# Kernel optimization log

Hardware: AMD Instinct MI355X
Metric: run time of the kernel (lower is better)

## Reference

```python
import jax, jax.numpy as jnp
import numpy as np

B, L, HID = 4, 4096, 1024
H, D = 16, 64  # num_heads, head_dim


def setup_inputs() -> dict:
    key = jax.random.key(0)
    ks = jax.random.split(key, 5)
    s = 1.0 / np.sqrt(HID)
    mk = lambda k: jax.random.uniform(k, (HID, HID), minval=-s, maxval=s, dtype=jnp.float32)
    return {
        "x": jax.random.normal(ks[0], (B, L, HID), dtype=jnp.float32),
        "Wq": mk(ks[1]), "bq": jnp.zeros((HID,), jnp.float32),
        "Wk": mk(ks[2]), "bk": jnp.zeros((HID,), jnp.float32),
        "Wv": mk(ks[3]), "bv": jnp.zeros((HID,), jnp.float32),
        "Wo": mk(ks[4]), "bo": jnp.zeros((HID,), jnp.float32),
    }


def reference(x, Wq, bq, Wk, bk, Wv, bv, Wo, bo):
    Bx, Lx, _ = x.shape
    # projections (weights stored [in, out])
    q = (x @ Wq + bq).reshape(Bx, Lx, H, D)
    k = (x @ Wk + bk).reshape(Bx, Lx, H, D)
    v = (x @ Wv + bv).reshape(Bx, Lx, H, D)
    # Single window (L <= window_size): torch matmul batches over (B, L) and
    # contracts head_dim -> per-token head-to-head scores [B, L, H, H].
    scores = jnp.einsum('blhd,bled->blhe', q, k) / np.sqrt(D).astype(np.float32)
    probs = jax.nn.softmax(scores, axis=-1)
    out = jnp.einsum('blhe,bled->blhd', probs, v).reshape(Bx, Lx, HID)
    return out @ Wo + bo
```

## Files before the change

### kernel.cpp

```cpp
#include <hip/hip_runtime.h>
#include <stdint.h>


typedef __attribute__((ext_vector_type(8))) short short8;
typedef __attribute__((ext_vector_type(4))) float floatx4;
typedef __attribute__((address_space(1))) unsigned int gu32;
typedef __attribute__((address_space(3))) unsigned int lu32;

#define HID 1024
#define MTOK 16384
#define WELEM (HID * HID)
#define XELEM (MTOK * HID)

#define SBAR() __builtin_amdgcn_s_barrier()
#define WAITLGKM() do { asm volatile("s_waitcnt lgkmcnt(0)" ::: "memory"); \
                        __builtin_amdgcn_sched_barrier(0); } while (0)
#define VMCNT(n) do { asm volatile("s_waitcnt vmcnt(" #n ")" ::: "memory"); \
                      __builtin_amdgcn_sched_barrier(0); } while (0)

__device__ __forceinline__ unsigned short f2bf(float f) {
  union { float f; uint32_t u; } v; v.f = f;
  uint32_t u = v.u;
  u += 0x7fffu + ((u >> 16) & 1u);
  return (unsigned short)(u >> 16);
}

__global__ __launch_bounds__(256) void cvt_x_kernel(const float* __restrict__ x,
                                                    unsigned short* __restrict__ xb) {
  const int idx = blockIdx.x * 256 + threadIdx.x;
  float4 v = ((const float4*)x)[idx];
  ushort4 o;
  o.x = f2bf(v.x); o.y = f2bf(v.y); o.z = f2bf(v.z); o.w = f2bf(v.w);
  ((ushort4*)xb)[idx] = o;
}

__global__ __launch_bounds__(256) void cvt_w_kernel(const float* __restrict__ W0,
                                                    const float* __restrict__ W1,
                                                    const float* __restrict__ W2,
                                                    const float* __restrict__ W3,
                                                    unsigned short* __restrict__ WT) {
  const float* W = (blockIdx.z == 0) ? W0 : (blockIdx.z == 1) ? W1
                   : (blockIdx.z == 2) ? W2 : W3;
  unsigned short* out = WT + (size_t)blockIdx.z * WELEM;
  __shared__ float tile[64][65];
  const int t = threadIdx.x;
  const int n0 = blockIdx.x * 64, k0 = blockIdx.y * 64;
#pragma unroll
  for (int i = 0; i < 4; i++) {
    const int row = i * 16 + (t >> 4);
    const int col = (t & 15) * 4;
    float4 v = *(const float4*)&W[(size_t)(k0 + row) * HID + n0 + col];
    tile[row][col] = v.x; tile[row][col + 1] = v.y;
    tile[row][col + 2] = v.z; tile[row][col + 3] = v.w;
  }
  __syncthreads();
#pragma unroll
  for (int i = 0; i < 4; i++) {
    const int n = i * 16 + (t >> 4);
    const int k = (t & 15) * 4;
    ushort4 o;
    o.x = f2bf(tile[k][n]);     o.y = f2bf(tile[k + 1][n]);
    o.z = f2bf(tile[k + 2][n]); o.w = f2bf(tile[k + 3][n]);
    *(ushort4*)&out[(size_t)(n0 + n) * HID + k0 + k] = o;
  }
}

template <bool QKV>
__global__ __launch_bounds__(512, 2) void gemm256(
    const unsigned short* __restrict__ A,
    const unsigned short* __restrict__ BTb,
    const float* __restrict__ b0, const float* __restrict__ b1,
    const float* __restrict__ b2,
    void* __restrict__ Cv)
{
  __shared__ short8 smem_[131072 / 16];
  char* smem = (char*)smem_;

  constexpr int R = QKV ? 3 : 1;
  const int bid = blockIdx.x;
  const int xcd = bid & 7;
  const int j = bid >> 3;
  const int nb0 = j >> 3;
  const int mb = xcd * 8 + (j & 7);
  const int m0 = mb * 256;
  const int cb = nb0 * 256;

  const unsigned short* BT0 = QKV ? BTb : (BTb + (size_t)3 * WELEM);

  const int t_ = threadIdx.x;
  const int wv = t_ >> 6, lane = t_ & 63;
  const int quad = lane >> 4, r16 = lane & 15;
  const int wm = wv >> 2, wn = wv & 3;

  const int srow = wv * 16 + (lane >> 2);
  const int scol = ((lane & 3) ^ ((lane >> 3) & 3)) * 8;
  const unsigned short* Ag = A + (size_t)(m0 + srow) * HID + scol;
  const unsigned short* Bg = BT0 + (size_t)(cb + srow) * HID + scol;

  const int qsw = (quad ^ ((r16 >> 1) & 3)) << 4;
  const char* Ard = smem + wm * 16384 + r16 * 64 + qsw;
  const char* Brd = smem + 32768 + (wn >> 1) * 16384 + ((wn & 1) * 64 + r16) * 64 + qsw;

  floatx4 acc[8][4] = {};

  auto stageA = [&](int h, int tt) {
    const unsigned short* s = Ag + (size_t)h * 128 * HID + tt * 64;
    char* d = smem + ((tt & 1) << 16) + h * 16384 + wv * 1024;
    __builtin_amdgcn_global_load_lds((const gu32*)s,        (lu32*)d,          16, 0, 0);
    __builtin_amdgcn_global_load_lds((const gu32*)(s + 32), (lu32*)(d + 8192), 16, 0, 0);
  };
  auto stageB = [&](int h, int tt) {
    const unsigned short* s = Bg + (size_t)h * 128 * HID + tt * 64;
    char* d = smem + ((tt & 1) << 16) + 32768 + h * 16384 + wv * 1024;
    __builtin_amdgcn_global_load_lds((const gu32*)s,        (lu32*)d,          16, 0, 0);
    __builtin_amdgcn_global_load_lds((const gu32*)(s + 32), (lu32*)(d + 8192), 16, 0, 0);
  };

  const int NT = HID / 64;

  short8 alo[4][2], ahi[4][2];
  short8 b01[2][2], b23[2][2];

  stageA(0, 0); stageA(1, 0); stageB(0, 0); stageB(1, 0);
  VMCNT(0);
  SBAR();
#pragma unroll
  for (int ks = 0; ks < 2; ++ks)
#pragma unroll
    for (int mi = 0; mi < 4; ++mi)
      alo[mi][ks] = *(const short8*)(Ard + ks * 8192 + mi * 1024);

  for (int r = 0; r < R; ++r) {
    for (int t = 0; t < NT; ++t) {
      const int bufb = (t & 1) << 16;
      const int nxtb = bufb ^ 0x10000;
      const bool more = (t + 1 < NT);

      if (more) { stageA(0, t + 1); VMCNT(2); } else { VMCNT(0); }
      SBAR();
#pragma unroll
      for (int ks = 0; ks < 2; ++ks)
#pragma unroll
        for (int ni = 0; ni < 2; ++ni)
          b01[ni][ks] = *(const short8*)(Brd + bufb + ks * 8192 + ni * 1024);
#pragma unroll
      for (int ks = 0; ks < 2; ++ks)
#pragma unroll
        for (int ni = 0; ni < 2; ++ni)
          b23[ni][ks] = *(const short8*)(Brd + bufb + ks * 8192 + (2 + ni) * 1024);
      __builtin_amdgcn_s_setprio(1);
#pragma unroll
      for (int ks = 0; ks < 2; ++ks)
#pragma unroll
        for (int mi = 0; mi < 4; ++mi)
#pragma unroll
          for (int ni = 0; ni < 2; ++ni)
            acc[mi][ni] = __builtin_amdgcn_mfma_f32_16x16x32_bf16(alo[mi][ks], b01[ni][ks], acc[mi][ni], 0, 0, 0);
      __builtin_amdgcn_s_setprio(0);
      WAITLGKM();

      if (more) stageA(1, t + 1);
      SBAR();
#pragma unroll
      for (int ks = 0; ks < 2; ++ks)
#pragma unroll
        for (int mi = 0; mi < 4; ++mi)
          ahi[mi][ks] = *(const short8*)(Ard + bufb + ks * 8192 + (4 + mi) * 1024);
      __builtin_amdgcn_s_setprio(1);
#pragma unroll
      for (int ks = 0; ks < 2; ++ks)
#pragma unroll
        for (int mi = 0; mi < 4; ++mi)
#pragma unroll
          for (int ni = 0; ni < 2; ++ni)
            acc[mi][2 + ni] = __builtin_amdgcn_mfma_f32_16x16x32_bf16(alo[mi][ks], b23[ni][ks], acc[mi][2 + ni], 0, 0, 0);
      __builtin_amdgcn_s_setprio(0);
      WAITLGKM();

      if (more) { stageB(0, t + 1); VMCNT(4); }
      SBAR();
      if (more) {
#pragma unroll
        for (int ks = 0; ks < 2; ++ks)
#pragma unroll
          for (int mi = 0; mi < 2; ++mi)
            alo[mi][ks] = *(const short8*)(Ard + nxtb + ks * 8192 + mi * 1024);
      }
      __builtin_amdgcn_s_setprio(1);
#pragma unroll
      for (int ks = 0; ks < 2; ++ks)
#pragma unroll
        for (int mi = 0; mi < 4; ++mi)
#pragma unroll
          for (int ni = 0; ni < 2; ++ni)
            acc[4 + mi][2 + ni] = __builtin_amdgcn_mfma_f32_16x16x32_bf16(ahi[mi][ks], b23[ni][ks], acc[4 + mi][2 + ni], 0, 0, 0);
      __builtin_amdgcn_s_setprio(0);
      WAITLGKM();

      if (more) stageB(1, t + 1);
      SBAR();
      if (more) {
#pragma unroll
        for (int ks = 0; ks < 2; ++ks)
#pragma unroll
          for (int mi = 2; mi < 4; ++mi)
            alo[mi][ks] = *(const short8*)(Ard + nxtb + ks * 8192 + mi * 1024);
      }
      __builtin_amdgcn_s_setprio(1);
#pragma unroll
      for (int ks = 0; ks < 2; ++ks)
#pragma unroll
        for (int mi = 0; mi < 4; ++mi)
#pragma unroll
          for (int ni = 0; ni < 2; ++ni)
            acc[4 + mi][ni] = __builtin_amdgcn_mfma_f32_16x16x32_bf16(ahi[mi][ks], b01[ni][ks], acc[4 + mi][ni], 0, 0, 0);
      __builtin_amdgcn_s_setprio(0);
      WAITLGKM();
    }

    if (r + 1 < R) {
      Bg += WELEM;
      stageA(0, 0); stageA(1, 0); stageB(0, 0); stageB(1, 0);
    }

    {
      const float* bias = QKV ? ((r == 0) ? b0 : ((r == 1) ? b1 : b2)) : b0;
      float bvv[4];
#pragma unroll
      for (int ni = 0; ni < 4; ++ni) bvv[ni] = bias[cb + wn * 64 + ni * 16 + r16];

      const int row0 = m0 + wm * 128 + quad * 4;
      unsigned short* outb = (unsigned short*)Cv + (size_t)r * XELEM;
      float* outf = (float*)Cv;
#pragma unroll
      for (int mi = 0; mi < 8; ++mi) {
#pragma unroll
        for (int rr = 0; rr < 4; ++rr) {
          const size_t roff = (size_t)(row0 + mi * 16 + rr) * HID + cb + wn * 64 + r16;
#pragma unroll
          for (int ni = 0; ni < 4; ++ni) {
            const float val = acc[mi][ni][rr] + bvv[ni];
            if constexpr (QKV) outb[roff + ni * 16] = f2bf(val);
            else               outf[roff + ni * 16] = val;
          }
        }
      }
    }

    if (r + 1 < R) {
#pragma unroll
      for (int mi = 0; mi < 8; ++mi)
#pragma unroll
        for (int ni = 0; ni < 4; ++ni)
          acc[mi][ni] = floatx4{0.f, 0.f, 0.f, 0.f};
      VMCNT(0);
      SBAR();
#pragma unroll
      for (int ks = 0; ks < 2; ++ks)
#pragma unroll
        for (int mi = 0; mi < 4; ++mi)
          alo[mi][ks] = *(const short8*)(Ard + ks * 8192 + mi * 1024);
    }
  }
}

__global__ __launch_bounds__(256) void attn_kernel(const unsigned short* qkv,
                                                   unsigned short* attn) {
  __shared__ unsigned short vls[4][1056];
  __shared__ unsigned short pls[4][16 * 24];

  const int t = threadIdx.x;
  const int wv = t >> 6, lane = t & 63;
  const int quad = lane >> 4, r16 = lane & 15;
  const size_t base = ((size_t)blockIdx.x * 4 + wv) * HID;
  const unsigned short* qp = qkv + base;
  const unsigned short* kp = qkv + (size_t)XELEM + base;
  const unsigned short* vp = qkv + 2 * (size_t)XELEM + base;

  __builtin_amdgcn_global_load_lds((const gu32*)(vp + lane * 8),       (lu32*)&vls[wv][0],   16, 0, 0);
  __builtin_amdgcn_global_load_lds((const gu32*)(vp + 512 + lane * 8), (lu32*)&vls[wv][528], 16, 0, 0);

  short8 qf0 = *(const short8*)(qp + r16 * 64 + quad * 8);
  short8 qf1 = *(const short8*)(qp + r16 * 64 + quad * 8 + 32);
  short8 kf0 = *(const short8*)(kp + r16 * 64 + quad * 8);
  short8 kf1 = *(const short8*)(kp + r16 * 64 + quad * 8 + 32);

  floatx4 sc = {0.f, 0.f, 0.f, 0.f};
  sc = __builtin_amdgcn_mfma_f32_16x16x32_bf16(qf0, kf0, sc, 0, 0, 0);
  sc = __builtin_amdgcn_mfma_f32_16x16x32_bf16(qf1, kf1, sc, 0, 0, 0);

#pragma unroll
  for (int rr = 0; rr < 4; rr++) {
    float s = sc[rr] * 0.125f;
    float m = s;
#pragma unroll
    for (int off = 1; off < 16; off <<= 1) m = fmaxf(m, __shfl_xor(m, off));
    float ex = __expf(s - m);
    float sum = ex;
#pragma unroll
    for (int off = 1; off < 16; off <<= 1) sum += __shfl_xor(sum, off);
    pls[wv][(quad * 4 + rr) * 24 + r16] = f2bf(ex / sum);
  }

  __syncthreads();

  const short8 zero8 = {0, 0, 0, 0, 0, 0, 0, 0};
  short8 af = zero8;
  short8 bf[4] = {zero8, zero8, zero8, zero8};
  if (quad < 2) {
    af = *(const short8*)&pls[wv][r16 * 24 + quad * 8];
#pragma unroll
    for (int c = 0; c < 4; c++)
#pragma unroll
      for (int jj = 0; jj < 8; jj++)
        bf[c][jj] = (short)vls[wv][quad * 528 + jj * 64 + c * 16 + r16];
  }

  floatx4 ov[4];
#pragma unroll
  for (int c = 0; c < 4; c++) {
    floatx4 z = {0.f, 0.f, 0.f, 0.f};
    ov[c] = __builtin_amdgcn_mfma_f32_16x16x32_bf16(af, bf[c], z, 0, 0, 0);
  }

#pragma unroll
  for (int rr = 0; rr < 4; rr++)
#pragma unroll
    for (int c = 0; c < 4; c++)
      attn[base + (size_t)(quad * 4 + rr) * 64 + c * 16 + r16] = f2bf(ov[c][rr]);
}

extern "C" void kernel_launch(void* const* d_in, const int* in_sizes, int n_in,
                              void* d_out, int out_size, void* d_ws, size_t ws_size,
                              hipStream_t stream) {
  const float* x  = (const float*)d_in[0];
  const float* Wq = (const float*)d_in[1];
  const float* bq = (const float*)d_in[2];
  const float* Wk = (const float*)d_in[3];
  const float* bk = (const float*)d_in[4];
  const float* Wv = (const float*)d_in[5];
  const float* bv = (const float*)d_in[6];
  const float* Wo = (const float*)d_in[7];
  const float* bo = (const float*)d_in[8];

  char* ws = (char*)d_ws;
  unsigned short* xb  = (unsigned short*)ws;
  unsigned short* wt  = (unsigned short*)(ws + (size_t)XELEM * 2);
  unsigned short* qkv = wt + 4 * (size_t)WELEM;

  cvt_x_kernel<<<XELEM / 1024, 256, 0, stream>>>(x, xb);
  cvt_w_kernel<<<dim3(16, 16, 4), 256, 0, stream>>>(Wq, Wk, Wv, Wo, wt);
  gemm256<true><<<256, 512, 0, stream>>>(xb, wt, bq, bk, bv, (void*)qkv);
  attn_kernel<<<4096, 256, 0, stream>>>(qkv, qkv);
  gemm256<false><<<256, 512, 0, stream>>>(qkv, wt, bo, bo, bo, d_out);
}
```

Before: 287.2 us.

## Simplify GEMM main loop to one barrier per K-tile with bulk prefetch

Replaces the four-phase ping-pong schedule in the GEMM loop with a simpler one. At the top of each K-tile it issues all global-to-LDS loads for the next tile, reads all A and B fragments for the current tile from LDS, and runs all 32 MFMAs. It then waits for the loads and uses a single barrier. This removes three barriers and the interleaved partial waits per tile, at the cost of less fine-grained overlap between LDS reads, prefetch and MFMA work, and higher register pressure from holding every fragment at once.

```diff
diff --git a/kernel.cpp b/kernel.cpp
--- a/kernel.cpp
+++ b/kernel.cpp
@@ -124,20 +124,20 @@
   stageA(0, 0); stageA(1, 0); stageB(0, 0); stageB(1, 0);
   VMCNT(0);
   SBAR();
-#pragma unroll
-  for (int ks = 0; ks < 2; ++ks)
-#pragma unroll
-    for (int mi = 0; mi < 4; ++mi)
-      alo[mi][ks] = *(const short8*)(Ard + ks * 8192 + mi * 1024);
 
   for (int r = 0; r < R; ++r) {
     for (int t = 0; t < NT; ++t) {
       const int bufb = (t & 1) << 16;
-      const int nxtb = bufb ^ 0x10000;
       const bool more = (t + 1 < NT);
 
-      if (more) { stageA(0, t + 1); VMCNT(2); } else { VMCNT(0); }
-      SBAR();
+      if (more) { stageA(0, t + 1); stageA(1, t + 1);
+                  stageB(0, t + 1); stageB(1, t + 1); }
+
+#pragma unroll
+      for (int ks = 0; ks < 2; ++ks)
+#pragma unroll
+        for (int mi = 0; mi < 4; ++mi)
+          alo[mi][ks] = *(const short8*)(Ard + bufb + ks * 8192 + mi * 1024);
 #pragma unroll
       for (int ks = 0; ks < 2; ++ks)
 #pragma unroll
@@ -148,6 +148,12 @@
 #pragma unroll
         for (int ni = 0; ni < 2; ++ni)
           b23[ni][ks] = *(const short8*)(Brd + bufb + ks * 8192 + (2 + ni) * 1024);
+#pragma unroll
+      for (int ks = 0; ks < 2; ++ks)
+#pragma unroll
+        for (int mi = 0; mi < 4; ++mi)
+          ahi[mi][ks] = *(const short8*)(Ard + bufb + ks * 8192 + (4 + mi) * 1024);
+
       __builtin_amdgcn_s_setprio(1);
 #pragma unroll
       for (int ks = 0; ks < 2; ++ks)
@@ -156,17 +162,6 @@
 #pragma unroll
           for (int ni = 0; ni < 2; ++ni)
             acc[mi][ni] = __builtin_amdgcn_mfma_f32_16x16x32_bf16(alo[mi][ks], b01[ni][ks], acc[mi][ni], 0, 0, 0);
-      __builtin_amdgcn_s_setprio(0);
-      WAITLGKM();
-
-      if (more) stageA(1, t + 1);
-      SBAR();
-#pragma unroll
-      for (int ks = 0; ks < 2; ++ks)
-#pragma unroll
-        for (int mi = 0; mi < 4; ++mi)
-          ahi[mi][ks] = *(const short8*)(Ard + bufb + ks * 8192 + (4 + mi) * 1024);
-      __builtin_amdgcn_s_setprio(1);
 #pragma unroll
       for (int ks = 0; ks < 2; ++ks)
 #pragma unroll
@@ -174,19 +169,6 @@
 #pragma unroll
           for (int ni = 0; ni < 2; ++ni)
             acc[mi][2 + ni] = __builtin_amdgcn_mfma_f32_16x16x32_bf16(alo[mi][ks], b23[ni][ks], acc[mi][2 + ni], 0, 0, 0);
-      __builtin_amdgcn_s_setprio(0);
-      WAITLGKM();
-
-      if (more) { stageB(0, t + 1); VMCNT(4); }
-      SBAR();
-      if (more) {
-#pragma unroll
-        for (int ks = 0; ks < 2; ++ks)
-#pragma unroll
-          for (int mi = 0; mi < 2; ++mi)
-            alo[mi][ks] = *(const short8*)(Ard + nxtb + ks * 8192 + mi * 1024);
-      }
-      __builtin_amdgcn_s_setprio(1);
 #pragma unroll
       for (int ks = 0; ks < 2; ++ks)
 #pragma unroll
@@ -194,19 +176,6 @@
 #pragma unroll
           for (int ni = 0; ni < 2; ++ni)
             acc[4 + mi][2 + ni] = __builtin_amdgcn_mfma_f32_16x16x32_bf16(ahi[mi][ks], b23[ni][ks], acc[4 + mi][2 + ni], 0, 0, 0);
-      __builtin_amdgcn_s_setprio(0);
-      WAITLGKM();
-
-      if (more) stageB(1, t + 1);
-      SBAR();
-      if (more) {
-#pragma unroll
-        for (int ks = 0; ks < 2; ++ks)
-#pragma unroll
-          for (int mi = 2; mi < 4; ++mi)
-            alo[mi][ks] = *(const short8*)(Ard + nxtb + ks * 8192 + mi * 1024);
-      }
-      __builtin_amdgcn_s_setprio(1);
 #pragma unroll
       for (int ks = 0; ks < 2; ++ks)
 #pragma unroll
@@ -215,7 +184,10 @@
           for (int ni = 0; ni < 2; ++ni)
             acc[4 + mi][ni] = __builtin_amdgcn_mfma_f32_16x16x32_bf16(ahi[mi][ks], b01[ni][ks], acc[4 + mi][ni], 0, 0, 0);
       __builtin_amdgcn_s_setprio(0);
+
       WAITLGKM();
+      VMCNT(0);
+      SBAR();
     }
 
     if (r + 1 < R) {
@@ -255,11 +227,6 @@
           acc[mi][ni] = floatx4{0.f, 0.f, 0.f, 0.f};
       VMCNT(0);
       SBAR();
-#pragma unroll
-      for (int ks = 0; ks < 2; ++ks)
-#pragma unroll
-        for (int mi = 0; mi < 4; ++mi)
-          alo[mi][ks] = *(const short8*)(Ard + ks * 8192 + mi * 1024);
     }
   }
 }
```

Result: slower. 296.3 us (+3.2%).
